# Kernel tuning notes

Hardware: AMD Instinct MI355X
Metric: run time of the kernel (lower is better)

Reference implementation:

```python
import jax, jax.numpy as jnp
import numpy as np

B, T, FDIM, H = 8, 2048, 512, 8
DK = FDIM // H
INF_VAL = 10000.0


def setup_inputs() -> dict:
    key = jax.random.key(0)
    ks = jax.random.split(key, 12)
    s = 1.0 / np.sqrt(FDIM)
    return {
        "query": jax.random.normal(ks[0], (B, T, FDIM), jnp.float32),
        "key": jax.random.normal(ks[1], (B, T, FDIM), jnp.float32),
        "value": jax.random.normal(ks[2], (B, T, FDIM), jnp.float32),
        "mask": jax.random.bernoulli(ks[3], 0.1, (B, T, T)),
        "Wq": jax.random.normal(ks[4], (FDIM, FDIM), jnp.float32) * s,
        "bq": jnp.zeros((FDIM,), jnp.float32),
        "Wk": jax.random.normal(ks[5], (FDIM, FDIM), jnp.float32) * s,
        "bk": jnp.zeros((FDIM,), jnp.float32),
        "Wv": jax.random.normal(ks[6], (FDIM, FDIM), jnp.float32) * s,
        "bv": jnp.zeros((FDIM,), jnp.float32),
        "Wo": jax.random.normal(ks[7], (FDIM, FDIM), jnp.float32) * s,
        "bo": jnp.zeros((FDIM,), jnp.float32),
    }


def reference(query, key, value, mask, Wq, bq, Wk, bk, Wv, bv, Wo, bo):
    # Linear projections (torch Linear: y = x W^T + b) then split heads.
    q = (query @ Wq.T + bq).reshape(B, T, H, DK).transpose(0, 2, 1, 3)  # (B,H,T1,DK)
    k = (key @ Wk.T + bk).reshape(B, T, H, DK).transpose(0, 2, 1, 3)    # (B,H,T2,DK)
    v = (value @ Wv.T + bv).reshape(B, T, H, DK).transpose(0, 2, 1, 3)  # (B,H,T2,DK)
    scores = jnp.einsum("bhqd,bhkd->bhqk", q, k) / jnp.sqrt(jnp.float32(DK))
    m = mask[:, None, :, :]  # (B,1,T1,T2)
    scores = jnp.where(m, -INF_VAL, scores)
    attn = jax.nn.softmax(scores, axis=-1)
    attn = jnp.where(m, 0.0, attn)
    # dropout_rate = 0.0 -> identity
    x = jnp.einsum("bhqk,bhkd->bhqd", attn, v)  # (B,H,T1,DK)
    x = x.transpose(0, 2, 1, 3).reshape(B, T, H * DK)
    return x @ Wo.T + bo
```

## Files before the change

kernel.cpp:

```cpp
#include <hip/hip_runtime.h>
#include <hip/hip_bf16.h>
#include <stdint.h>

#define B_N 8
#define T_N 2048
#define FDIM_N 512
#define H_N 8
#define DK_N 64

typedef float f32x4 __attribute__((ext_vector_type(4)));
typedef float float4v __attribute__((ext_vector_type(4)));
typedef __bf16 bf16x8 __attribute__((ext_vector_type(8)));
typedef unsigned short ushort8v __attribute__((ext_vector_type(8)));
typedef unsigned int uint2v __attribute__((ext_vector_type(2)));
typedef unsigned int uint4v __attribute__((ext_vector_type(4)));

#if __has_builtin(__builtin_amdgcn_exp2f)
#define EXP2F(x) __builtin_amdgcn_exp2f(x)
#else
#define EXP2F(x) exp2f(x)
#endif

static __device__ __forceinline__ unsigned short f2bf(float f) {
  unsigned int u = __builtin_bit_cast(unsigned int, f);
  u += 0x7fffu + ((u >> 16) & 1u);
  return (unsigned short)(u >> 16);
}

static __device__ __forceinline__ unsigned cvtpk(float lo, float hi) {
  unsigned r;
  asm("v_cvt_pk_bf16_f32 %0, %1, %2" : "=v"(r) : "v"(lo), "v"(hi));
  return r;
}

static __device__ __forceinline__ void gld_lds16(const void* g, void* l) {
  __builtin_amdgcn_global_load_lds(
      (const __attribute__((address_space(1))) unsigned int*)g,
      (__attribute__((address_space(3))) unsigned int*)l, 16, 0, 0);
}

static __device__ __forceinline__ bf16x8 ld_bf8(const unsigned short* p) {
  return *reinterpret_cast<const bf16x8*>(p);
}

#define SWZ8(row, colE) ((colE) ^ (((row) & 7) << 3))

#define QSCALE 0.1803368801111244f

__global__ __launch_bounds__(256) void prep_k(
    const int* __restrict__ m, const float* __restrict__ w0, const float* __restrict__ w1,
    const float* __restrict__ w2, const float* __restrict__ w3,
    const float* __restrict__ qin, const float* __restrict__ kin, const float* __restrict__ vin,
    unsigned short* __restrict__ wb, unsigned short* __restrict__ qb,
    unsigned short* __restrict__ kb, unsigned short* __restrict__ vb,
    unsigned long long* __restrict__ mbits) {
  const int bid = blockIdx.x;
  if (bid < 2048) {
    const size_t n = (size_t)B_N * T_N * T_N;
    const size_t stride = (size_t)2048 * 256;
    for (size_t i = (size_t)bid * 256 + threadIdx.x; i < n; i += stride) {
      unsigned long long bl = __ballot(m[i] != 0);
      if ((threadIdx.x & 63) == 0) mbits[i >> 6] = bl;
    }
  } else if (bid < 2560) {
    const int i = (bid - 2048) * 256 + threadIdx.x;
    const int ws = i >> 15, o = i & 32767;
    const float* w = (ws == 0) ? w0 : (ws == 1) ? w1 : (ws == 2) ? w2 : w3;
    const float4v a = *reinterpret_cast<const float4v*>(w + (size_t)o * 8);
    const float4v b = *reinterpret_cast<const float4v*>(w + (size_t)o * 8 + 4);
    const ushort8v out = {f2bf(a.x), f2bf(a.y), f2bf(a.z), f2bf(a.w),
                          f2bf(b.x), f2bf(b.y), f2bf(b.z), f2bf(b.w)};
    *reinterpret_cast<ushort8v*>(wb + (size_t)i * 8) = out;
  } else {
    const unsigned total = 3u << 20;
    const unsigned stride = 1536u * 256u;
    for (unsigned i = (bid - 2560) * 256 + threadIdx.x; i < total; i += stride) {
      const unsigned sel = i >> 20, off = i & 0xFFFFFu;
      const float* in = (sel == 0) ? qin : (sel == 1) ? kin : vin;
      unsigned short* out = (sel == 0) ? qb : (sel == 1) ? kb : vb;
      const float4v a = *reinterpret_cast<const float4v*>(in + (size_t)off * 8);
      const float4v b = *reinterpret_cast<const float4v*>(in + (size_t)off * 8 + 4);
      const ushort8v o = {f2bf(a.x), f2bf(a.y), f2bf(a.z), f2bf(a.w),
                          f2bf(b.x), f2bf(b.y), f2bf(b.z), f2bf(b.w)};
      *reinterpret_cast<ushort8v*>(out + (size_t)off * 8) = o;
    }
  }
}

template <int MODE>
__global__ __launch_bounds__(256, 3) void gemm_bt_k(const unsigned short* __restrict__ Ap,
                                                    const unsigned short* __restrict__ Wp,
                                                    const float* __restrict__ biasp,
                                                    void* __restrict__ Cp) {
  __shared__ unsigned short As[128 * 64];
  __shared__ unsigned short Bs[128 * 64];
  const int tid = threadIdx.x;
  const int lane = tid & 63, w = tid >> 6;
  const int lr = lane & 15, lg = lane >> 4;
  const int id = blockIdx.x;
  const int work = (id & 7) * 64 + (id >> 3);
  const int m0 = (work >> 2) * 128, n0 = (work & 3) * 128;
  const int wm = (w & 1) * 64, wn = (w >> 1) * 64;
  const int swz_rd = (lr & 7) << 3;

  f32x4 acc[4][4];
  const f32x4 z4 = {0.f, 0.f, 0.f, 0.f};
#pragma unroll
  for (int i = 0; i < 4; ++i)
#pragma unroll
    for (int j = 0; j < 4; ++j) acc[i][j] = z4;

  for (int k0 = 0; k0 < 512; k0 += 64) {
    __syncthreads();
#pragma unroll
    for (int i = 0; i < 4; ++i) {
      const int c = i * 256 + tid;
      const int row = c >> 3, ch = c & 7;
      const int sw = SWZ8(row, ch * 8);
      gld_lds16(Ap + (size_t)(m0 + row) * 512 + k0 + sw, &As[c * 8]);
      gld_lds16(Wp + (size_t)(n0 + row) * 512 + k0 + sw, &Bs[c * 8]);
    }
    __syncthreads();
    bf16x8 af[4][2], bw[4][2];
#pragma unroll
    for (int mt = 0; mt < 4; ++mt)
#pragma unroll
      for (int kk = 0; kk < 2; ++kk)
        af[mt][kk] = ld_bf8(&As[(wm + mt * 16 + lr) * 64 + ((kk * 32 + lg * 8) ^ swz_rd)]);
#pragma unroll
    for (int nt = 0; nt < 4; ++nt)
#pragma unroll
      for (int kk = 0; kk < 2; ++kk)
        bw[nt][kk] = ld_bf8(&Bs[(wn + nt * 16 + lr) * 64 + ((kk * 32 + lg * 8) ^ swz_rd)]);
#pragma unroll
    for (int kk = 0; kk < 2; ++kk)
#pragma unroll
      for (int mt = 0; mt < 4; ++mt)
#pragma unroll
        for (int nt = 0; nt < 4; ++nt)
          acc[mt][nt] =
              __builtin_amdgcn_mfma_f32_16x16x32_bf16(af[mt][kk], bw[nt][kk], acc[mt][nt], 0, 0, 0);
  }

#pragma unroll
  for (int nt = 0; nt < 4; ++nt) {
    const int n = n0 + wn + nt * 16 + lr;
    const float bias = biasp[n];
#pragma unroll
    for (int mt = 0; mt < 4; ++mt) {
#pragma unroll
      for (int j = 0; j < 4; ++j) {
        const int m = m0 + wm + mt * 16 + lg * 4 + j;
        float v = acc[mt][nt][j] + bias;
        const int bb = m >> 11, t = m & 2047;
        const int hh = n >> 6, d = n & 63;
        if constexpr (MODE == 0) {
          v *= QSCALE;
          ((unsigned short*)Cp)[(((size_t)(bb * 8 + hh) * 2048 + t) << 6) + d] = f2bf(v);
        } else if constexpr (MODE == 1) {
          ((unsigned short*)Cp)[(((size_t)(bb * 8 + hh) * 2048 + t) << 6) + d] = f2bf(v);
        } else if constexpr (MODE == 2) {
          const int tp = (t & ~31) | (((t >> 2) & 3) << 3) | (((t >> 4) & 1) << 2) | (t & 3);
          ((unsigned short*)Cp)[(((size_t)(bb * 8 + hh) * 64 + d) << 11) + tp] = f2bf(v);
        } else {
          ((float*)Cp)[(size_t)m * 512 + n] = v;
        }
      }
    }
  }
}

__global__ __launch_bounds__(512, 4) void attn_k(
    const unsigned short* __restrict__ qg, const unsigned short* __restrict__ kg,
    const unsigned short* __restrict__ vtg, const unsigned long long* __restrict__ mb,
    unsigned short* __restrict__ xg) {
  __shared__ unsigned short L[4 * 8192];

  const int tid = threadIdx.x;
  const int lane = tid & 63, w = tid >> 6;
  const int lr = lane & 15, lg = lane >> 4;
  const int swz_rd = (lr & 7) << 3;
  const int id = blockIdx.x;
  const int work = (id & 7) * 128 + (id >> 3);
  const int bh = work >> 4, qt0 = work & 15;
  const int b = bh >> 3, h = bh & 7;
  const int q0 = qt0 * 128;

  bf16x8 aq[2];
#pragma unroll
  for (int kk = 0; kk < 2; ++kk)
    aq[kk] = ld_bf8(qg + ((size_t)bh * T_N + q0 + w * 16 + lr) * DK_N + kk * 32 + lg * 8);

  const unsigned short* rp[8];
#pragma unroll
  for (int st = 0; st < 4; ++st) {
    rp[2 * st + 0] = &L[(st * 16 + lr) * 64 + ((lg * 8) ^ swz_rd)];
    rp[2 * st + 1] = &L[(st * 16 + lr) * 64 + ((32 + lg * 8) ^ swz_rd)];
  }

  const int krow = tid >> 3, kch = tid & 7;
  const unsigned short* kp =
      kg + (size_t)bh * (T_N * DK_N) + krow * 64 + SWZ8(krow, kch * 8);
  const unsigned short* vp =
      vtg + ((size_t)bh * DK_N + krow) * T_N + SWZ8(krow, kch * 8);
  const unsigned long long* mp = mb + ((size_t)b * T_N + q0 + w * 16 + lr) * (T_N / 64);

  f32x4 OT[4];
  float rsacc = 0.f;
  const f32x4 z4 = {0.f, 0.f, 0.f, 0.f};
#pragma unroll
  for (int dt = 0; dt < 4; ++dt) OT[dt] = z4;

  f32x4 ST[4];
  bf16x8 pfrag[2];
  unsigned long long mA, mB;

#define STG(B_)                                       \
  {                                                   \
    gld_lds16(kp, &L[(B_) * 8192 + tid * 8]);         \
    gld_lds16(vp, &L[(B_) * 8192 + 4096 + tid * 8]);  \
    kp += 4096; vp += 64;                             \
  }

#define QKT(B_)                                                                             \
  {                                                                                         \
    __builtin_amdgcn_s_setprio(1);                                                          \
    _Pragma("unroll") for (int st = 0; st < 4; ++st) {                                      \
      const bf16x8 kb0 = ld_bf8(rp[2 * st + 0] + (B_) * 8192);                              \
      const bf16x8 kb1 = ld_bf8(rp[2 * st + 1] + (B_) * 8192);                              \
      f32x4 a_ = __builtin_amdgcn_mfma_f32_16x16x32_bf16(kb0, aq[0], z4, 0, 0, 0);          \
      ST[st] = __builtin_amdgcn_mfma_f32_16x16x32_bf16(kb1, aq[1], a_, 0, 0, 0);            \
    }                                                                                       \
    __builtin_amdgcn_s_setprio(0);                                                          \
  }

#define SM(MREG)                                                                            \
  {                                                                                         \
    float sv[4][4];                                                                         \
    _Pragma("unroll") for (int st = 0; st < 4; ++st) {                                      \
      const unsigned nib = (unsigned)((MREG) >> (st * 16 + lg * 4)) & 0xFu;                 \
      _Pragma("unroll") for (int j = 0; j < 4; ++j) {                                       \
        float e = EXP2F(ST[st][j]);                                                         \
        e = ((nib >> j) & 1u) ? 0.f : e;                                                    \
        sv[st][j] = e;                                                                      \
      }                                                                                     \
    }                                                                                       \
    rsacc += (((sv[0][0] + sv[0][1]) + (sv[0][2] + sv[0][3])) +                             \
              ((sv[1][0] + sv[1][1]) + (sv[1][2] + sv[1][3]))) +                            \
             (((sv[2][0] + sv[2][1]) + (sv[2][2] + sv[2][3])) +                             \
              ((sv[3][0] + sv[3][1]) + (sv[3][2] + sv[3][3])));                             \
    uint4v pk0_, pk1_;                                                                      \
    pk0_.x = cvtpk(sv[0][0], sv[0][1]); pk0_.y = cvtpk(sv[0][2], sv[0][3]);                 \
    pk0_.z = cvtpk(sv[1][0], sv[1][1]); pk0_.w = cvtpk(sv[1][2], sv[1][3]);                 \
    pk1_.x = cvtpk(sv[2][0], sv[2][1]); pk1_.y = cvtpk(sv[2][2], sv[2][3]);                 \
    pk1_.z = cvtpk(sv[3][0], sv[3][1]); pk1_.w = cvtpk(sv[3][2], sv[3][3]);                 \
    pfrag[0] = __builtin_bit_cast(bf16x8, pk0_);                                            \
    pfrag[1] = __builtin_bit_cast(bf16x8, pk1_);                                            \
  }

#define PV(B_)                                                                              \
  {                                                                                         \
    __builtin_amdgcn_s_setprio(1);                                                          \
    _Pragma("unroll") for (int dt = 0; dt < 4; ++dt) {                                      \
      const bf16x8 v0 = ld_bf8(rp[2 * dt + 0] + (B_) * 8192 + 4096);                        \
      const bf16x8 v1 = ld_bf8(rp[2 * dt + 1] + (B_) * 8192 + 4096);                        \
      f32x4 o_ = __builtin_amdgcn_mfma_f32_16x16x32_bf16(v0, pfrag[0], OT[dt], 0, 0, 0);    \
      OT[dt] = __builtin_amdgcn_mfma_f32_16x16x32_bf16(v1, pfrag[1], o_, 0, 0, 0);          \
    }                                                                                       \
    __builtin_amdgcn_s_setprio(0);                                                          \
  }

  STG(0); STG(1);
  mA = mp[0]; mB = mp[1];
  const unsigned long long* mload = mp + 3;
  __syncthreads();
  QKT(0); STG(2); SM(mA); mA = mp[2];

#define ITER2A                                                              \
  {                                                                                         \
    PV(0); __syncthreads();                                                                 \
    QKT(1); STG(3); SM(mB); mB = mload[0];                                                  \
    PV(1);                                                                                  \
    QKT(2); STG(0); SM(mA); mA = mload[1]; mload += 2;                                      \
  }
#define ITER2B                                                              \
  {                                                                                         \
    PV(2); __syncthreads();                                                                 \
    QKT(3); STG(1); SM(mB); mB = mload[0];                                                  \
    PV(3);                                                                                  \
    QKT(0); STG(2); SM(mA); mA = mload[1]; mload += 2;                                      \
  }

  for (int i = 0; i < 7; ++i) {
    ITER2A;
    ITER2B;
  }
  {
    PV(0); __syncthreads();
    QKT(1); STG(3); SM(mB); mB = mload[0];
    PV(1);
    QKT(2); SM(mA);
  }
  PV(2);
  __syncthreads();
  QKT(3); SM(mB);
  PV(3);
#undef ITER2A
#undef ITER2B
#undef STG
#undef QKT
#undef SM
#undef PV

  {
    float l = rsacc;
    l += __shfl_xor(l, 16);
    l += __shfl_xor(l, 32);
    const float inv = (l > 0.f) ? 1.f / l : 0.f;
    const int q = q0 + w * 16 + lr;
#pragma unroll
    for (int dt = 0; dt < 4; ++dt) {
      uint2v o;
      o.x = cvtpk(OT[dt][0] * inv, OT[dt][1] * inv);
      o.y = cvtpk(OT[dt][2] * inv, OT[dt][3] * inv);
      *reinterpret_cast<uint2v*>(xg + ((size_t)(b * T_N + q)) * FDIM_N + h * 64 + dt * 16 +
                                 lg * 4) = o;
    }
  }
}

extern "C" void kernel_launch(void* const* d_in, const int* in_sizes, int n_in,
                              void* d_out, int out_size, void* d_ws, size_t ws_size,
                              hipStream_t stream) {
  const float* query = (const float*)d_in[0];
  const float* key = (const float*)d_in[1];
  const float* value = (const float*)d_in[2];
  const int* mask = (const int*)d_in[3];
  const float* Wq = (const float*)d_in[4];
  const float* bq = (const float*)d_in[5];
  const float* Wk = (const float*)d_in[6];
  const float* bk = (const float*)d_in[7];
  const float* Wv = (const float*)d_in[8];
  const float* bv = (const float*)d_in[9];
  const float* Wo = (const float*)d_in[10];
  const float* bo = (const float*)d_in[11];

  const size_t NE = (size_t)16384 * 512;
  const size_t WE = (size_t)512 * 512;
  unsigned short* qb_in = (unsigned short*)d_ws;
  unsigned short* kb_in = qb_in + NE;
  unsigned short* vb_in = kb_in + NE;
  unsigned short* wqb = vb_in + NE;
  unsigned short* q_scr = wqb + 4 * WE;
  unsigned short* k_scr = q_scr + NE;
  unsigned short* vT_scr = k_scr + NE;
  unsigned long long* mbits = (unsigned long long*)(vT_scr + NE);
  unsigned short* x_scr = qb_in;

  prep_k<<<4096, 256, 0, stream>>>(mask, Wq, Wk, Wv, Wo, query, key, value, wqb, qb_in, kb_in,
                                   vb_in, mbits);
  gemm_bt_k<0><<<512, 256, 0, stream>>>(qb_in, wqb + 0 * WE, bq, q_scr);
  gemm_bt_k<1><<<512, 256, 0, stream>>>(kb_in, wqb + 1 * WE, bk, k_scr);
  gemm_bt_k<2><<<512, 256, 0, stream>>>(vb_in, wqb + 2 * WE, bv, vT_scr);
  attn_k<<<1024, 512, 0, stream>>>(q_scr, k_scr, vT_scr, mbits, x_scr);
  gemm_bt_k<3><<<512, 256, 0, stream>>>(x_scr, wqb + 3 * WE, bo, (float*)d_out);
}
```

Before: 213.7 us.

## Process two 16-row query tiles per wave to reuse K/V LDS fragments

Each wave now handles 32 query rows (two 16-row subtiles) instead of 16, so the attention block covers 256 queries and the grid halves to 512 blocks. Every K and V fragment read from LDS feeds two MFMAs, which halves LDS read traffic and global K/V staging per query. The cost is doubled accumulator, score and mask registers, which may cut occupancy under the existing launch bounds. Fewer blocks (512 on 256 CUs) also lowers wave-level parallelism and tail balance.

```diff
diff --git a/kernel.cpp b/kernel.cpp
--- a/kernel.cpp
+++ b/kernel.cpp
@@ -181,15 +181,18 @@
   const int lr = lane & 15, lg = lane >> 4;
   const int swz_rd = (lr & 7) << 3;
   const int id = blockIdx.x;
-  const int work = (id & 7) * 128 + (id >> 3);
-  const int bh = work >> 4, qt0 = work & 15;
+  const int work = (id & 7) * 64 + (id >> 3);
+  const int bh = work >> 3, qt0 = work & 7;
   const int b = bh >> 3, h = bh & 7;
-  const int q0 = qt0 * 128;
-
-  bf16x8 aq[2];
-#pragma unroll
-  for (int kk = 0; kk < 2; ++kk)
-    aq[kk] = ld_bf8(qg + ((size_t)bh * T_N + q0 + w * 16 + lr) * DK_N + kk * 32 + lg * 8);
+  const int q0 = qt0 * 256;
+
+  bf16x8 aq[2][2];
+#pragma unroll
+  for (int qt = 0; qt < 2; ++qt)
+#pragma unroll
+    for (int kk = 0; kk < 2; ++kk)
+      aq[qt][kk] =
+          ld_bf8(qg + ((size_t)bh * T_N + q0 + w * 32 + qt * 16 + lr) * DK_N + kk * 32 + lg * 8);
 
   const unsigned short* rp[8];
 #pragma unroll
@@ -203,17 +206,20 @@
       kg + (size_t)bh * (T_N * DK_N) + krow * 64 + SWZ8(krow, kch * 8);
   const unsigned short* vp =
       vtg + ((size_t)bh * DK_N + krow) * T_N + SWZ8(krow, kch * 8);
-  const unsigned long long* mp = mb + ((size_t)b * T_N + q0 + w * 16 + lr) * (T_N / 64);
-
-  f32x4 OT[4];
-  float rsacc = 0.f;
+  const unsigned long long* mpA = mb + ((size_t)b * T_N + q0 + w * 32 + lr) * (T_N / 64);
+  const unsigned long long* mpB = mpA + 16 * (T_N / 64);
+
+  f32x4 OT[2][4];
+  float rsacc[2] = {0.f, 0.f};
   const f32x4 z4 = {0.f, 0.f, 0.f, 0.f};
 #pragma unroll
-  for (int dt = 0; dt < 4; ++dt) OT[dt] = z4;
-
-  f32x4 ST[4];
-  bf16x8 pfrag[2];
-  unsigned long long mA, mB;
+  for (int qt = 0; qt < 2; ++qt)
+#pragma unroll
+    for (int dt = 0; dt < 4; ++dt) OT[qt][dt] = z4;
+
+  f32x4 ST[2][4];
+  bf16x8 pfrag[2][2];
+  unsigned long long mA0, mA1, mB0, mB1;
 
 #define STG(B_)                                       \
   {                                                   \
@@ -228,34 +234,39 @@
     _Pragma("unroll") for (int st = 0; st < 4; ++st) {                                      \
       const bf16x8 kb0 = ld_bf8(rp[2 * st + 0] + (B_) * 8192);                              \
       const bf16x8 kb1 = ld_bf8(rp[2 * st + 1] + (B_) * 8192);                              \
-      f32x4 a_ = __builtin_amdgcn_mfma_f32_16x16x32_bf16(kb0, aq[0], z4, 0, 0, 0);          \
-      ST[st] = __builtin_amdgcn_mfma_f32_16x16x32_bf16(kb1, aq[1], a_, 0, 0, 0);            \
+      _Pragma("unroll") for (int qt = 0; qt < 2; ++qt) {                                    \
+        f32x4 a_ = __builtin_amdgcn_mfma_f32_16x16x32_bf16(kb0, aq[qt][0], z4, 0, 0, 0);    \
+        ST[qt][st] = __builtin_amdgcn_mfma_f32_16x16x32_bf16(kb1, aq[qt][1], a_, 0, 0, 0);  \
+      }                                                                                     \
     }                                                                                       \
     __builtin_amdgcn_s_setprio(0);                                                          \
   }
 
-#define SM(MREG)                                                                            \
-  {                                                                                         \
-    float sv[4][4];                                                                         \
-    _Pragma("unroll") for (int st = 0; st < 4; ++st) {                                      \
-      const unsigned nib = (unsigned)((MREG) >> (st * 16 + lg * 4)) & 0xFu;                 \
-      _Pragma("unroll") for (int j = 0; j < 4; ++j) {                                       \
-        float e = EXP2F(ST[st][j]);                                                         \
-        e = ((nib >> j) & 1u) ? 0.f : e;                                                    \
-        sv[st][j] = e;                                                                      \
+#define SM(M0_, M1_)                                                                        \
+  {                                                                                         \
+    _Pragma("unroll") for (int qt = 0; qt < 2; ++qt) {                                      \
+      const unsigned long long mrow = qt ? (M1_) : (M0_);                                   \
+      float sv[4][4];                                                                       \
+      _Pragma("unroll") for (int st = 0; st < 4; ++st) {                                    \
+        const unsigned nib = (unsigned)(mrow >> (st * 16 + lg * 4)) & 0xFu;                 \
+        _Pragma("unroll") for (int j = 0; j < 4; ++j) {                                     \
+          float e = EXP2F(ST[qt][st][j]);                                                   \
+          e = ((nib >> j) & 1u) ? 0.f : e;                                                  \
+          sv[st][j] = e;                                                                    \
+        }                                                                                   \
       }                                                                                     \
+      rsacc[qt] += (((sv[0][0] + sv[0][1]) + (sv[0][2] + sv[0][3])) +                       \
+                    ((sv[1][0] + sv[1][1]) + (sv[1][2] + sv[1][3]))) +                      \
+                   (((sv[2][0] + sv[2][1]) + (sv[2][2] + sv[2][3])) +                       \
+                    ((sv[3][0] + sv[3][1]) + (sv[3][2] + sv[3][3])));                       \
+      uint4v pk0_, pk1_;                                                                    \
+      pk0_.x = cvtpk(sv[0][0], sv[0][1]); pk0_.y = cvtpk(sv[0][2], sv[0][3]);               \
+      pk0_.z = cvtpk(sv[1][0], sv[1][1]); pk0_.w = cvtpk(sv[1][2], sv[1][3]);               \
+      pk1_.x = cvtpk(sv[2][0], sv[2][1]); pk1_.y = cvtpk(sv[2][2], sv[2][3]);               \
+      pk1_.z = cvtpk(sv[3][0], sv[3][1]); pk1_.w = cvtpk(sv[3][2], sv[3][3]);               \
+      pfrag[qt][0] = __builtin_bit_cast(bf16x8, pk0_);                                      \
+      pfrag[qt][1] = __builtin_bit_cast(bf16x8, pk1_);                                      \
     }                                                                                       \
-    rsacc += (((sv[0][0] + sv[0][1]) + (sv[0][2] + sv[0][3])) +                             \
-              ((sv[1][0] + sv[1][1]) + (sv[1][2] + sv[1][3]))) +                            \
-             (((sv[2][0] + sv[2][1]) + (sv[2][2] + sv[2][3])) +                             \
-              ((sv[3][0] + sv[3][1]) + (sv[3][2] + sv[3][3])));                             \
-    uint4v pk0_, pk1_;                                                                      \
-    pk0_.x = cvtpk(sv[0][0], sv[0][1]); pk0_.y = cvtpk(sv[0][2], sv[0][3]);                 \
-    pk0_.z = cvtpk(sv[1][0], sv[1][1]); pk0_.w = cvtpk(sv[1][2], sv[1][3]);                 \
-    pk1_.x = cvtpk(sv[2][0], sv[2][1]); pk1_.y = cvtpk(sv[2][2], sv[2][3]);                 \
-    pk1_.z = cvtpk(sv[3][0], sv[3][1]); pk1_.w = cvtpk(sv[3][2], sv[3][3]);                 \
-    pfrag[0] = __builtin_bit_cast(bf16x8, pk0_);                                            \
-    pfrag[1] = __builtin_bit_cast(bf16x8, pk1_);                                            \
   }
 
 #define PV(B_)                                                                              \
@@ -264,31 +275,38 @@
     _Pragma("unroll") for (int dt = 0; dt < 4; ++dt) {                                      \
       const bf16x8 v0 = ld_bf8(rp[2 * dt + 0] + (B_) * 8192 + 4096);                        \
       const bf16x8 v1 = ld_bf8(rp[2 * dt + 1] + (B_) * 8192 + 4096);                        \
-      f32x4 o_ = __builtin_amdgcn_mfma_f32_16x16x32_bf16(v0, pfrag[0], OT[dt], 0, 0, 0);    \
-      OT[dt] = __builtin_amdgcn_mfma_f32_16x16x32_bf16(v1, pfrag[1], o_, 0, 0, 0);          \
+      _Pragma("unroll") for (int qt = 0; qt < 2; ++qt) {                                    \
+        f32x4 o_ =                                                                          \
+            __builtin_amdgcn_mfma_f32_16x16x32_bf16(v0, pfrag[qt][0], OT[qt][dt], 0, 0, 0); \
+        OT[qt][dt] = __builtin_amdgcn_mfma_f32_16x16x32_bf16(v1, pfrag[qt][1], o_, 0, 0, 0);\
+      }                                                                                     \
     }                                                                                       \
     __builtin_amdgcn_s_setprio(0);                                                          \
   }
 
   STG(0); STG(1);
-  mA = mp[0]; mB = mp[1];
-  const unsigned long long* mload = mp + 3;
+  mA0 = mpA[0]; mA1 = mpB[0];
+  mB0 = mpA[1]; mB1 = mpB[1];
+  const unsigned long long* mloadA = mpA + 3;
+  const unsigned long long* mloadB = mpB + 3;
   __syncthreads();
-  QKT(0); STG(2); SM(mA); mA = mp[2];
-
-#define ITER2A                                                              \
+  QKT(0); STG(2); SM(mA0, mA1); mA0 = mpA[2]; mA1 = mpB[2];
+
+#define ITER2A                                                                              \
   {                                                                                         \
     PV(0); __syncthreads();                                                                 \
-    QKT(1); STG(3); SM(mB); mB = mload[0];                                                  \
+    QKT(1); STG(3); SM(mB0, mB1); mB0 = mloadA[0]; mB1 = mloadB[0];                         \
     PV(1);                                                                                  \
-    QKT(2); STG(0); SM(mA); mA = mload[1]; mload += 2;                                      \
-  }
-#define ITER2B                                                              \
+    QKT(2); STG(0); SM(mA0, mA1); mA0 = mloadA[1]; mA1 = mloadB[1];                         \
+    mloadA += 2; mloadB += 2;                                                               \
+  }
+#define ITER2B                                                                              \
   {                                                                                         \
     PV(2); __syncthreads();                                                                 \
-    QKT(3); STG(1); SM(mB); mB = mload[0];                                                  \
+    QKT(3); STG(1); SM(mB0, mB1); mB0 = mloadA[0]; mB1 = mloadB[0];                         \
     PV(3);                                                                                  \
-    QKT(0); STG(2); SM(mA); mA = mload[1]; mload += 2;                                      \
+    QKT(0); STG(2); SM(mA0, mA1); mA0 = mloadA[1]; mA1 = mloadB[1];                         \
+    mloadA += 2; mloadB += 2;                                                               \
   }
 
   for (int i = 0; i < 7; ++i) {
@@ -297,13 +315,13 @@
   }
   {
     PV(0); __syncthreads();
-    QKT(1); STG(3); SM(mB); mB = mload[0];
+    QKT(1); STG(3); SM(mB0, mB1); mB0 = mloadA[0]; mB1 = mloadB[0];
     PV(1);
-    QKT(2); SM(mA);
+    QKT(2); SM(mA0, mA1);
   }
   PV(2);
   __syncthreads();
-  QKT(3); SM(mB);
+  QKT(3); SM(mB0, mB1);
   PV(3);
 #undef ITER2A
 #undef ITER2B
@@ -312,17 +330,18 @@
 #undef SM
 #undef PV
 
-  {
-    float l = rsacc;
+#pragma unroll
+  for (int qt = 0; qt < 2; ++qt) {
+    float l = rsacc[qt];
     l += __shfl_xor(l, 16);
     l += __shfl_xor(l, 32);
     const float inv = (l > 0.f) ? 1.f / l : 0.f;
-    const int q = q0 + w * 16 + lr;
+    const int q = q0 + w * 32 + qt * 16 + lr;
 #pragma unroll
     for (int dt = 0; dt < 4; ++dt) {
       uint2v o;
-      o.x = cvtpk(OT[dt][0] * inv, OT[dt][1] * inv);
-      o.y = cvtpk(OT[dt][2] * inv, OT[dt][3] * inv);
+      o.x = cvtpk(OT[qt][dt][0] * inv, OT[qt][dt][1] * inv);
+      o.y = cvtpk(OT[qt][dt][2] * inv, OT[qt][dt][3] * inv);
       *reinterpret_cast<uint2v*>(xg + ((size_t)(b * T_N + q)) * FDIM_N + h * 64 + dt * 16 +
                                  lg * 4) = o;
     }
@@ -362,6 +381,6 @@
   gemm_bt_k<0><<<512, 256, 0, stream>>>(qb_in, wqb + 0 * WE, bq, q_scr);
   gemm_bt_k<1><<<512, 256, 0, stream>>>(kb_in, wqb + 1 * WE, bk, k_scr);
   gemm_bt_k<2><<<512, 256, 0, stream>>>(vb_in, wqb + 2 * WE, bv, vT_scr);
-  attn_k<<<1024, 512, 0, stream>>>(q_scr, k_scr, vT_scr, mbits, x_scr);
+  attn_k<<<512, 512, 0, stream>>>(q_scr, k_scr, vT_scr, mbits, x_scr);
   gemm_bt_k<3><<<512, 256, 0, stream>>>(x_scr, wqb + 3 * WE, bo, (float*)d_out);
 }
```

New measurement: 245.3 us. 1.15x slower.

## Restructure attention loop to process two KV tiles per barrier with double score buffers

Applied to the files above, without the earlier changes.

Reorganizes the flash-attention main loop so each phase computes QK^T for two KV tiles into separate score register sets, issues staging for the next two tiles, then runs softmax and PV for both. This halves the number of workgroup barriers and batches MFMA work so the independent QK^T products can overlap exp/softmax math. The cost is more live registers (two score buffers plus prefetched mask words), which may reduce occupancy, and less fine-grained overlap between the LDS staging and compute than the previous staggered schedule.

```diff
diff --git a/kernel.cpp b/kernel.cpp
--- a/kernel.cpp
+++ b/kernel.cpp
@@ -211,9 +211,9 @@
 #pragma unroll
   for (int dt = 0; dt < 4; ++dt) OT[dt] = z4;
 
-  f32x4 ST[4];
+  f32x4 STa[4], STb[4];
   bf16x8 pfrag[2];
-  unsigned long long mA, mB;
+  unsigned long long mA, mB, mnA, mnB;
 
 #define STG(B_)                                       \
   {                                                   \
@@ -222,25 +222,25 @@
     kp += 4096; vp += 64;                             \
   }
 
-#define QKT(B_)                                                                             \
+#define QKT(B_, ST_)                                                                        \
   {                                                                                         \
     __builtin_amdgcn_s_setprio(1);                                                          \
     _Pragma("unroll") for (int st = 0; st < 4; ++st) {                                      \
       const bf16x8 kb0 = ld_bf8(rp[2 * st + 0] + (B_) * 8192);                              \
       const bf16x8 kb1 = ld_bf8(rp[2 * st + 1] + (B_) * 8192);                              \
       f32x4 a_ = __builtin_amdgcn_mfma_f32_16x16x32_bf16(kb0, aq[0], z4, 0, 0, 0);          \
-      ST[st] = __builtin_amdgcn_mfma_f32_16x16x32_bf16(kb1, aq[1], a_, 0, 0, 0);            \
+      ST_[st] = __builtin_amdgcn_mfma_f32_16x16x32_bf16(kb1, aq[1], a_, 0, 0, 0);           \
     }                                                                                       \
     __builtin_amdgcn_s_setprio(0);                                                          \
   }
 
-#define SM(MREG)                                                                            \
+#define SM(ST_, MREG)                                                                       \
   {                                                                                         \
     float sv[4][4];                                                                         \
     _Pragma("unroll") for (int st = 0; st < 4; ++st) {                                      \
       const unsigned nib = (unsigned)((MREG) >> (st * 16 + lg * 4)) & 0xFu;                 \
       _Pragma("unroll") for (int j = 0; j < 4; ++j) {                                       \
-        float e = EXP2F(ST[st][j]);                                                         \
+        float e = EXP2F(ST_[st][j]);                                                        \
         e = ((nib >> j) & 1u) ? 0.f : e;                                                    \
         sv[st][j] = e;                                                                      \
       }                                                                                     \
@@ -272,41 +272,36 @@
 
   STG(0); STG(1);
   mA = mp[0]; mB = mp[1];
-  const unsigned long long* mload = mp + 3;
+  const unsigned long long* mload = mp + 2;
   __syncthreads();
-  QKT(0); STG(2); SM(mA); mA = mp[2];
-
-#define ITER2A                                                              \
-  {                                                                                         \
-    PV(0); __syncthreads();                                                                 \
-    QKT(1); STG(3); SM(mB); mB = mload[0];                                                  \
-    PV(1);                                                                                  \
-    QKT(2); STG(0); SM(mA); mA = mload[1]; mload += 2;                                      \
-  }
-#define ITER2B                                                              \
-  {                                                                                         \
-    PV(2); __syncthreads();                                                                 \
-    QKT(3); STG(1); SM(mB); mB = mload[0];                                                  \
-    PV(3);                                                                                  \
-    QKT(0); STG(2); SM(mA); mA = mload[1]; mload += 2;                                      \
-  }
 
   for (int i = 0; i < 7; ++i) {
-    ITER2A;
-    ITER2B;
-  }
-  {
-    PV(0); __syncthreads();
-    QKT(1); STG(3); SM(mB); mB = mload[0];
-    PV(1);
-    QKT(2); SM(mA);
-  }
-  PV(2);
+    QKT(0, STa); QKT(1, STb);
+    STG(2); STG(3);
+    mnA = mload[0]; mnB = mload[1];
+    SM(STa, mA); PV(0);
+    SM(STb, mB); PV(1);
+    mA = mnA; mB = mnB;
+    __syncthreads();
+    QKT(2, STa); QKT(3, STb);
+    STG(0); STG(1);
+    mnA = mload[2]; mnB = mload[3];
+    SM(STa, mA); PV(2);
+    SM(STb, mB); PV(3);
+    mA = mnA; mB = mnB;
+    mload += 4;
+    __syncthreads();
+  }
+  QKT(0, STa); QKT(1, STb);
+  STG(2); STG(3);
+  mnA = mload[0]; mnB = mload[1];
+  SM(STa, mA); PV(0);
+  SM(STb, mB); PV(1);
+  mA = mnA; mB = mnB;
   __syncthreads();
-  QKT(3); SM(mB);
-  PV(3);
-#undef ITER2A
-#undef ITER2B
+  QKT(2, STa); QKT(3, STb);
+  SM(STa, mA); PV(2);
+  SM(STb, mB); PV(3);
 #undef STG
 #undef QKT
 #undef SM
```

New measurement: 213.9 us. Within noise of the previous version (+0.1%).
